# Kernel tuning notes

Measured on AMD Instinct MI355X. Metric: run time of the kernel, lower is better.

Reference implementation:

```python
import jax, jax.numpy as jnp
import numpy as np

D_MODEL, D_STATE, BATCH, SEQ = 512, 32, 8, 4096

def _hippo(n):
    i = np.arange(n)[:, None].astype(np.float64)
    j = np.arange(n)[None, :].astype(np.float64)
    P = np.where(i > j, np.sqrt(2 * i + 1) * np.sqrt(2 * j + 1), 0.0)
    P = P + np.diag(np.arange(1, n + 1).astype(np.float64))
    return (-P).astype(np.float32)

def setup_inputs() -> dict:
    key = jax.random.key(0)
    k0, k1, k2, k3 = jax.random.split(key, 4)
    x = jax.random.normal(k0, (BATCH, SEQ, D_MODEL), dtype=jnp.float32)
    A = jnp.asarray(_hippo(D_STATE))
    B = jax.random.normal(k1, (D_STATE, D_MODEL), dtype=jnp.float32) / np.float32(np.sqrt(D_MODEL))
    C = jax.random.normal(k2, (D_MODEL, D_STATE), dtype=jnp.float32) / np.float32(np.sqrt(D_STATE))
    D = jnp.ones((D_MODEL,), dtype=jnp.float32)
    log_dt = jnp.zeros((D_MODEL,), dtype=jnp.float32)
    W_out = jax.random.normal(k3, (D_MODEL, D_MODEL), dtype=jnp.float32) / np.float32(np.sqrt(D_MODEL))
    b_out = jnp.zeros((D_MODEL,), dtype=jnp.float32)
    return {"x": x, "A": A, "B": B, "C": C, "D": D, "log_dt": log_dt, "W_out": W_out, "b_out": b_out}

def reference(x, A, B, C, D, log_dt, W_out, b_out):
    # x: (b, s, d). S4 layer with bilinear discretization and tanh recurrence.
    n = A.shape[0]
    dt = jnp.mean(jnp.clip(jnp.exp(log_dt), 1e-4, 1.0))  # scalar dt.mean()
    I = jnp.eye(n, dtype=x.dtype)
    inv_term = jnp.linalg.inv(I - 0.5 * dt * A)
    A_bar = (I + 0.5 * dt * A) @ inv_term          # (n, n)
    B_bar = dt * (inv_term @ B)                    # (n, d)
    # Precompute input projection for all timesteps (vectorized):
    uB = jnp.einsum('bsd,nd->bsn', x, B_bar)       # (b, s, n)
    s0 = jnp.zeros((x.shape[0], n), dtype=x.dtype)
    def step(state, ub_t):
        state = jnp.tanh(state @ A_bar.T + ub_t)   # (b, n)
        return state, state
    final_state, states = jax.lax.scan(step, s0, jnp.swapaxes(uB, 0, 1))
    states = jnp.swapaxes(states, 0, 1)            # (b, s, n)
    y = jnp.einsum('bsn,dn->bsd', states, C) + x * D
    y = y @ W_out.T + b_out                        # output_proj (dropout = eval identity)
    return y, final_state
```

## Files before the change

### kernel.cpp

```cpp
#include <hip/hip_runtime.h>
#include <hip/hip_bf16.h>

#define D_MODEL 512
#define D_STATE 32
#define BATCH 8
#define SEQ 4096
#define MROWS (BATCH * SEQ)

typedef __bf16 bf16;
typedef __bf16 bf16x4 __attribute__((ext_vector_type(4)));
typedef __bf16 bf16x8 __attribute__((ext_vector_type(8)));
typedef float f32x4 __attribute__((ext_vector_type(4)));

#define CHUNK 16
#define BURN 80
#define NCHUNK (SEQ / CHUNK)

__device__ __forceinline__ bf16x8 cvt8(const f32x4 a, const f32x4 b) {
  bf16x8 h;
  h[0] = (bf16)a[0]; h[1] = (bf16)a[1]; h[2] = (bf16)a[2]; h[3] = (bf16)a[3];
  h[4] = (bf16)b[0]; h[5] = (bf16)b[1]; h[6] = (bf16)b[2]; h[7] = (bf16)b[3];
  return h;
}

__global__ __launch_bounds__(256) void k_pre(
    const float* __restrict__ A, const float* __restrict__ C, const float* __restrict__ Dv,
    const float* __restrict__ log_dt, const float* __restrict__ W,
    float* __restrict__ A_bar, float* __restrict__ XTs,
    bf16* __restrict__ CW, bf16* __restrict__ WD) {
  __shared__ float Xs[32][32];
  const int bid = blockIdx.x, t = threadIdx.x;
  float* Xf = &Xs[0][0];

  if (bid == 0) {
    {
      float v0 = __expf(log_dt[t]);
      float v1 = __expf(log_dt[t + 256]);
      v0 = fminf(fmaxf(v0, 1e-4f), 1.0f);
      v1 = fminf(fmaxf(v1, 1e-4f), 1.0f);
      Xf[t] = v0 + v1;
    }
    __syncthreads();
    for (int s2 = 128; s2 > 0; s2 >>= 1) {
      if (t < s2) Xf[t] += Xf[t + s2];
      __syncthreads();
    }
    const float dtv = Xf[0] * (1.0f / 512.0f);
    __syncthreads();
    {
      const int i0 = 4 * t;
      const f32x4 av = *(const f32x4*)(A + i0);
      f32x4 mv;
#pragma unroll
      for (int q = 0; q < 4; q++) {
        const int r = (i0 + q) >> 5, c = (i0 + q) & 31;
        mv[q] = (r == c ? 1.0f : 0.0f) - 0.5f * dtv * av[q];
      }
      *(f32x4*)(Xf + i0) = mv;
    }
    __syncthreads();
    if (t < 32) {
      const int j = t;
      float xcol[32];
#pragma unroll
      for (int i = 0; i < 32; i++) {
        float s0 = 0.f, s1 = 0.f, s2 = 0.f, s3 = 0.f;
#pragma unroll
        for (int k = 0; k < 32; k += 4) {
          if (k < i)     s0 -= Xf[i * 32 + k]     * xcol[k];
          if (k + 1 < i) s1 -= Xf[i * 32 + k + 1] * xcol[k + 1];
          if (k + 2 < i) s2 -= Xf[i * 32 + k + 2] * xcol[k + 2];
          if (k + 3 < i) s3 -= Xf[i * 32 + k + 3] * xcol[k + 3];
        }
        const float num = (i == j ? 1.0f : 0.0f) + ((s0 + s1) + (s2 + s3));
        xcol[i] = (i >= j) ? num / Xf[i * 32 + i] : 0.0f;
      }
#pragma unroll
      for (int i = 0; i < 32; i++) Xs[i][j] = xcol[i];
    }
    __syncthreads();
    {
      const int i0 = 4 * t;
      const int r = t >> 3;
      f32x4 ov;
#pragma unroll
      for (int q = 0; q < 4; q++) {
        const int c = (i0 + q) & 31;
        float s = 0.f;
#pragma unroll
        for (int k = 0; k < 32; k++) {
          const float p2 = (r == k ? 1.0f : 0.0f) + 0.5f * dtv * A[r * 32 + k];
          s = fmaf(p2, Xf[k * 32 + c], s);
        }
        ov[q] = s;
      }
      *(f32x4*)(A_bar + i0) = ov;
    }
#pragma unroll
    for (int i = 0; i < 4; i++) {
      const int idx = t + i * 256;
      const int k = idx >> 5, n = idx & 31;
      XTs[idx] = dtv * Xf[n * 32 + k];
    }
  } else if (bid <= 16) {
    const int w = t >> 6, lane = t & 63;
    const int l15 = lane & 15, kg = lane >> 4;
    const int m = w & 1, nf = w >> 1;
    const int eb = (bid - 1) * 32;
    const float* wp = W + (long)(eb + m * 16 + l15) * D_MODEL + kg * 8;
    const int ncol = nf * 16 + l15;
    f32x4 acc = (f32x4)(0.0f);
#pragma unroll 1
    for (int kt = 0; kt < 16; kt++) {
      const f32x4 w0 = *(const f32x4*)(wp + kt * 32);
      const f32x4 w1 = *(const f32x4*)(wp + kt * 32 + 4);
      const bf16x8 af = cvt8(w0, w1);
      bf16x8 bf;
#pragma unroll
      for (int j = 0; j < 8; j++)
        bf[j] = (bf16)C[(kt * 32 + kg * 8 + j) * D_STATE + ncol];
      acc = __builtin_amdgcn_mfma_f32_16x16x32_bf16(af, bf, acc, 0, 0, 0);
    }
#pragma unroll
    for (int jj = 0; jj < 4; jj++)
      CW[(eb + m * 16 + kg * 4 + jj) * D_STATE + ncol] = (bf16)acc[jj];
  } else {
#pragma unroll
    for (int jj = 0; jj < 16; jj++) {
      const int i = (bid - 17) * 16384 + jj * 1024 + t * 4;
      const f32x4 wv = *(const f32x4*)(W + i);
      const f32x4 dv = *(const f32x4*)(Dv + (i & 511));
      bf16x4 h;
#pragma unroll
      for (int q = 0; q < 4; q++) h[q] = (bf16)(wv[q] * dv[q]);
      *(bf16x4*)(WD + i) = h;
    }
  }
}

__device__ __forceinline__ void stage_x(const float* __restrict__ x, long rowbase,
                                        int kt, void* lds, int t) {
#pragma unroll
  for (int j = 0; j < 2; j++) {
    const int boff = j * 4096 + t * 16;
    const int r = boff >> 7;
    const int s = (boff >> 4) & 7;
    const int cb = (s ^ (r & 7)) << 4;
    const char* src = (const char*)(x + (rowbase + r) * D_MODEL) + kt * 128 + cb;
    const int udst = j * 4096 + ((t >> 6) << 10);
    __builtin_amdgcn_global_load_lds(
        (const __attribute__((address_space(1))) void*)src,
        (__attribute__((address_space(3))) void*)((char*)lds + udst), 16, 0, 0);
  }
}

__global__ __launch_bounds__(256, 2) void k_uB(
    const float* __restrict__ x, const float* __restrict__ B,
    const float* __restrict__ XTs,
    float* __restrict__ uB, bf16* __restrict__ xb) {
  __shared__ float xs[2][64 * 32];
  __shared__ float sXT[1024];
  __shared__ float srw[64 * 33];
  const int t = threadIdx.x, w = t >> 6, lane = t & 63;
  const int l15 = lane & 15, kg = lane >> 4;
  const long rowbase = (long)blockIdx.x * 64;

#pragma unroll
  for (int i = 0; i < 4; i++) sXT[t + i * 256] = XTs[t + i * 256];

  const int arow = w * 16 + l15;
  bf16* xo = xb + (rowbase + arow) * D_MODEL + kg * 8;
  const float* bp0 = B + l15 * D_MODEL + kg * 8;
  const float* bp1 = B + (16 + l15) * D_MODEL + kg * 8;
  const int ps0 = (((kg * 2) ^ (arow & 7)) << 2);
  const int ps1 = (((kg * 2 + 1) ^ (arow & 7)) << 2);
  const float* xsrow0 = &xs[0][arow * 32];
  const float* xsrow1 = &xs[1][arow * 32];

  f32x4 acc0 = (f32x4)(0.0f), acc1 = (f32x4)(0.0f);
  f32x4 cb0, cb1, cb2, cb3, nb0, nb1, nb2, nb3;

  stage_x(x, rowbase, 0, &xs[0][0], t);
  cb0 = *(const f32x4*)(bp0); cb1 = *(const f32x4*)(bp0 + 4);
  cb2 = *(const f32x4*)(bp1); cb3 = *(const f32x4*)(bp1 + 4);

#pragma unroll 1
  for (int kt = 0; kt < 16; kt++) {
    __syncthreads();
    if (kt < 15) {
      stage_x(x, rowbase, kt + 1, &xs[(kt + 1) & 1][0], t);
      const int o = (kt + 1) * 32;
      nb0 = *(const f32x4*)(bp0 + o); nb1 = *(const f32x4*)(bp0 + o + 4);
      nb2 = *(const f32x4*)(bp1 + o); nb3 = *(const f32x4*)(bp1 + o + 4);
    }
    const float* xr = (kt & 1) ? xsrow1 : xsrow0;
    const f32x4 a0 = *(const f32x4*)(xr + ps0);
    const f32x4 a1 = *(const f32x4*)(xr + ps1);
    const bf16x8 af = cvt8(a0, a1);
    *(bf16x8*)(xo + kt * 32) = af;
    const bf16x8 bh0 = cvt8(cb0, cb1);
    const bf16x8 bh1 = cvt8(cb2, cb3);
    bf16x8 bl0, bl1;
#pragma unroll
    for (int q = 0; q < 4; q++) {
      bl0[q]     = (bf16)(cb0[q] - (float)bh0[q]);
      bl0[q + 4] = (bf16)(cb1[q] - (float)bh0[q + 4]);
      bl1[q]     = (bf16)(cb2[q] - (float)bh1[q]);
      bl1[q + 4] = (bf16)(cb3[q] - (float)bh1[q + 4]);
    }
    acc0 = __builtin_amdgcn_mfma_f32_16x16x32_bf16(af, bh0, acc0, 0, 0, 0);
    acc0 = __builtin_amdgcn_mfma_f32_16x16x32_bf16(af, bl0, acc0, 0, 0, 0);
    acc1 = __builtin_amdgcn_mfma_f32_16x16x32_bf16(af, bh1, acc1, 0, 0, 0);
    acc1 = __builtin_amdgcn_mfma_f32_16x16x32_bf16(af, bl1, acc1, 0, 0, 0);
    cb0 = nb0; cb1 = nb1; cb2 = nb2; cb3 = nb3;
  }
#pragma unroll
  for (int jj = 0; jj < 4; jj++) {
    srw[(w * 16 + kg * 4 + jj) * 33 + l15]      = acc0[jj];
    srw[(w * 16 + kg * 4 + jj) * 33 + 16 + l15] = acc1[jj];
  }
  __syncthreads();
  {
    const int r = t & 63, ng = t >> 6;
    f32x4 u0 = (f32x4)(0.0f), u1 = (f32x4)(0.0f);
#pragma unroll
    for (int k = 0; k < 32; k++) {
      const float sv = srw[r * 33 + k];
      const f32x4 x0 = *(const f32x4*)&sXT[k * 32 + ng * 4];
      const f32x4 x1 = *(const f32x4*)&sXT[k * 32 + ng * 4 + 16];
#pragma unroll
      for (int q = 0; q < 4; q++) {
        u0[q] = fmaf(sv, x0[q], u0[q]);
        u1[q] = fmaf(sv, x1[q], u1[q]);
      }
    }
    float* up = uB + (rowbase + r) * D_STATE;
    *(f32x4*)(up + ng * 4) = u0;
    *(f32x4*)(up + ng * 4 + 16) = u1;
  }
}

__global__ void k_scan(const float* __restrict__ uB, const float* __restrict__ A_bar,
                       bf16* __restrict__ Sb, float* __restrict__ fs) {
  __shared__ float sbuf[256];
  const int t = threadIdx.x;
  const int g = t >> 5, n = t & 31;
  const int chain = blockIdx.x * 8 + g;
  const int b = chain >> 8;
  const int ch = chain & 255;
  const int cs = ch * CHUNK;
  const int t0 = cs - BURN;
  const int ce = cs + CHUNK;

  float a[32];
#pragma unroll
  for (int k = 0; k < 32; k += 4) {
    const f32x4 v = *(const f32x4*)(A_bar + n * 32 + k);
    a[k] = v[0]; a[k + 1] = v[1]; a[k + 2] = v[2]; a[k + 3] = v[3];
  }
#pragma unroll
  for (int k = 0; k < 32; k++) asm volatile("" : "+v"(a[k]));

  const float* ub = uB + (long)b * SEQ * D_STATE + n;
  bf16* sp = Sb + ((long)b * SEQ + cs) * D_STATE + n;
  float* myslot = &sbuf[g * 32];

  float s = 0.f;
  float ubuf[8], unext[8];
#pragma unroll
  for (int i = 0; i < 8; i++) {
    const int tt = t0 + i;
    ubuf[i] = (tt >= 0) ? ub[(long)tt * D_STATE] : 0.f;
  }
  for (int tg = t0; tg < ce; tg += 8) {
    const int tn = tg + 8;
#pragma unroll
    for (int i = 0; i < 8; i++) {
      const int tt = tn + i;
      unext[i] = (tt >= 0 && tt < ce) ? ub[(long)tt * D_STATE] : 0.f;
    }
#pragma unroll
    for (int i = 0; i < 8; i++) {
      const int tt = tg + i;
      myslot[n] = s;
      const f32x4 s0 = *(const f32x4*)(myslot + 0);
      const f32x4 s1 = *(const f32x4*)(myslot + 4);
      const f32x4 s2 = *(const f32x4*)(myslot + 8);
      const f32x4 s3 = *(const f32x4*)(myslot + 12);
      const f32x4 s4 = *(const f32x4*)(myslot + 16);
      const f32x4 s5 = *(const f32x4*)(myslot + 20);
      const f32x4 s6 = *(const f32x4*)(myslot + 24);
      const f32x4 s7 = *(const f32x4*)(myslot + 28);
      float acc0 = ubuf[i], acc1 = 0.f, acc2 = 0.f, acc3 = 0.f;
#pragma unroll
      for (int q = 0; q < 4; q++) {
        acc0 = fmaf(a[0 + q],  s0[q], acc0);
        acc1 = fmaf(a[4 + q],  s1[q], acc1);
        acc2 = fmaf(a[8 + q],  s2[q], acc2);
        acc3 = fmaf(a[12 + q], s3[q], acc3);
        acc0 = fmaf(a[16 + q], s4[q], acc0);
        acc1 = fmaf(a[20 + q], s5[q], acc1);
        acc2 = fmaf(a[24 + q], s6[q], acc2);
        acc3 = fmaf(a[28 + q], s7[q], acc3);
      }
      const float z = (acc0 + acc1) + (acc2 + acc3);
      const float e = __expf(2.f * z);
      const float r = __builtin_amdgcn_rcpf(e + 1.f);
      s = fmaf(-2.f, r, 1.f);
      if (tt >= cs) sp[(long)(tt - cs) * D_STATE] = (bf16)s;
    }
#pragma unroll
    for (int i = 0; i < 8; i++) ubuf[i] = unext[i];
  }
  if (ch == NCHUNK - 1) fs[b * D_STATE + n] = s;
}

__device__ __forceinline__ void stage_tile(const void* gbase, long row0, long rowStrideB,
                                           int kByte, void* lds, int w, int lane) {
#pragma unroll
  for (int j = 0; j < 2; j++) {
    const int base_off = (w << 11) + (j << 10);
    const int boff = base_off + (lane << 4);
    const int r = boff >> 6;
    const int s = (boff >> 4) & 3;
    const int cb = ((s ^ (r & 3)) << 4);
    const char* src = (const char*)gbase + (row0 + r) * rowStrideB + kByte + cb;
    __builtin_amdgcn_global_load_lds(
        (const __attribute__((address_space(1))) void*)src,
        (__attribute__((address_space(3))) void*)((char*)lds + base_off), 16, 0, 0);
  }
}

__global__ __launch_bounds__(256) void k_out(const bf16* __restrict__ xb,
                                             const bf16* __restrict__ WD,
                                             const bf16* __restrict__ Sb,
                                             const bf16* __restrict__ CW,
                                             const float* __restrict__ bias,
                                             float* __restrict__ out) {
  __shared__ bf16 As[2][128 * 32];
  __shared__ bf16 Bs[2][128 * 32];
  const int tid = threadIdx.x;
  const int w = tid >> 6, lane = tid & 63;
  const int swz = (blockIdx.x & 7) * 128 + (blockIdx.x >> 3);
  const int bm = swz >> 2, bn = swz & 3;
  const long rowbase = (long)bm * 128;
  const long colbase = (long)bn * 128;
  const int wr = w >> 1, wc = w & 1;
  const int l15 = lane & 15, kg = lane >> 4;
  const int kgs = kg ^ (l15 & 3);

  f32x4 acc[4][4];
#pragma unroll
  for (int m = 0; m < 4; m++)
#pragma unroll
    for (int n = 0; n < 4; n++) acc[m][n] = (f32x4)(0.0f);

  const int aoff = (wr * 64 + l15) * 32 + kgs * 8;
  const int boff = (wc * 64 + l15) * 32 + kgs * 8;

  auto STAGE = [&](int ti, int b) {
    if (ti < 16) {
      stage_tile(xb, rowbase, 1024, ti * 64, &As[b][0], w, lane);
      stage_tile(WD, colbase, 1024, ti * 64, &Bs[b][0], w, lane);
    } else {
      stage_tile(Sb, rowbase, 64, 0, &As[b][0], w, lane);
      stage_tile(CW, colbase, 64, 0, &Bs[b][0], w, lane);
    }
  };

  STAGE(0, 0);
  __syncthreads();
#pragma unroll 1
  for (int kt = 0; kt < 17; kt++) {
    const int cur = kt & 1;
    if (kt < 16) STAGE(kt + 1, cur ^ 1);
    bf16x8 af[4], bfr[4];
#pragma unroll
    for (int m = 0; m < 4; m++) af[m] = *(const bf16x8*)&As[cur][aoff + m * 16 * 32];
#pragma unroll
    for (int n = 0; n < 4; n++) bfr[n] = *(const bf16x8*)&Bs[cur][boff + n * 16 * 32];
#pragma unroll
    for (int m = 0; m < 4; m++)
#pragma unroll
      for (int n = 0; n < 4; n++)
        acc[m][n] = __builtin_amdgcn_mfma_f32_16x16x32_bf16(af[m], bfr[n], acc[m][n], 0, 0, 0);
    __syncthreads();
  }
#pragma unroll
  for (int n = 0; n < 4; n++) {
    const int e = (int)colbase + wc * 64 + n * 16 + l15;
    const float bv = bias[e];
#pragma unroll
    for (int m = 0; m < 4; m++) {
      const long r0 = rowbase + wr * 64 + m * 16 + kg * 4;
      const f32x4 v = acc[m][n];
#pragma unroll
      for (int jj = 0; jj < 4; jj++) out[(r0 + jj) * (long)D_MODEL + e] = v[jj] + bv;
    }
  }
}

extern "C" void kernel_launch(void* const* d_in, const int* in_sizes, int n_in,
                              void* d_out, int out_size, void* d_ws, size_t ws_size,
                              hipStream_t stream) {
  const float* x      = (const float*)d_in[0];
  const float* A      = (const float*)d_in[1];
  const float* B      = (const float*)d_in[2];
  const float* C      = (const float*)d_in[3];
  const float* Dv     = (const float*)d_in[4];
  const float* log_dt = (const float*)d_in[5];
  const float* W      = (const float*)d_in[6];
  const float* b_out  = (const float*)d_in[7];
  float* out = (float*)d_out;
  float* fs  = out + (long)MROWS * D_MODEL;

  char* ws = (char*)d_ws;
  float* A_bar = (float*)(ws + 0);
  float* XTs   = (float*)(ws + (4L << 10));
  bf16*  CW    = (bf16*)(ws + (68L << 10));
  bf16*  WD    = (bf16*)(ws + (100L << 10));
  bf16*  Sb    = (bf16*)(ws + (612L << 10));
  float* uB    = (float*)(ws + (2660L << 10));
  bf16*  xb    = (bf16*)(ws + (6756L << 10));

  k_pre<<<dim3(33), dim3(256), 0, stream>>>(A, C, Dv, log_dt, W, A_bar, XTs, CW, WD);
  k_uB<<<dim3(MROWS / 64), dim3(256), 0, stream>>>(x, B, XTs, uB, xb);
  k_scan<<<dim3(256), dim3(256), 0, stream>>>(uB, A_bar, Sb, fs);
  k_out<<<dim3((MROWS / 128) * (D_MODEL / 128)), dim3(256), 0, stream>>>(xb, WD, Sb, CW, b_out, out);
}
```

Baseline: 91.22 us.

## Use fp16 dot2 in scan, widen output GEMM tile, raise uB occupancy

The scan kernel now keeps A_bar and the shared state in fp16 and uses packed fdot2 instructions, which halves the LDS traffic and the FMA count per recurrence step. The output GEMM tile grows from 128x128 to 128x256 per block to improve operand reuse, at the cost of more accumulator registers and fewer blocks. k_uB launch bounds now request 4 blocks per CU. The fp16 state and A_bar values lower the precision of the tanh recurrence.

```diff
diff --git a/kernel.cpp b/kernel.cpp
--- a/kernel.cpp
+++ b/kernel.cpp
@@ -11,6 +11,9 @@
 typedef __bf16 bf16x4 __attribute__((ext_vector_type(4)));
 typedef __bf16 bf16x8 __attribute__((ext_vector_type(8)));
 typedef float f32x4 __attribute__((ext_vector_type(4)));
+typedef _Float16 half_t;
+typedef _Float16 half2_t __attribute__((ext_vector_type(2)));
+typedef _Float16 half8 __attribute__((ext_vector_type(8)));
 
 #define CHUNK 16
 #define BURN 80
@@ -154,7 +157,7 @@
   }
 }
 
-__global__ __launch_bounds__(256, 2) void k_uB(
+__global__ __launch_bounds__(256, 4) void k_uB(
     const float* __restrict__ x, const float* __restrict__ B,
     const float* __restrict__ XTs,
     float* __restrict__ uB, bf16* __restrict__ xb) {
@@ -242,7 +245,7 @@
 
 __global__ void k_scan(const float* __restrict__ uB, const float* __restrict__ A_bar,
                        bf16* __restrict__ Sb, float* __restrict__ fs) {
-  __shared__ float sbuf[256];
+  __shared__ half_t hs[256];
   const int t = threadIdx.x;
   const int g = t >> 5, n = t & 31;
   const int chain = blockIdx.x * 8 + g;
@@ -252,18 +255,18 @@
   const int t0 = cs - BURN;
   const int ce = cs + CHUNK;
 
-  float a[32];
-#pragma unroll
-  for (int k = 0; k < 32; k += 4) {
-    const f32x4 v = *(const f32x4*)(A_bar + n * 32 + k);
-    a[k] = v[0]; a[k + 1] = v[1]; a[k + 2] = v[2]; a[k + 3] = v[3];
-  }
-#pragma unroll
-  for (int k = 0; k < 32; k++) asm volatile("" : "+v"(a[k]));
+  half2_t ah[16];
+#pragma unroll
+  for (int k = 0; k < 16; k++) {
+    ah[k][0] = (half_t)A_bar[n * 32 + 2 * k];
+    ah[k][1] = (half_t)A_bar[n * 32 + 2 * k + 1];
+  }
+#pragma unroll
+  for (int k = 0; k < 16; k++) asm volatile("" : "+v"(ah[k]));
 
   const float* ub = uB + (long)b * SEQ * D_STATE + n;
   bf16* sp = Sb + ((long)b * SEQ + cs) * D_STATE + n;
-  float* myslot = &sbuf[g * 32];
+  half_t* myslot = &hs[g * 32];
 
   float s = 0.f;
   float ubuf[8], unext[8];
@@ -282,27 +285,32 @@
 #pragma unroll
     for (int i = 0; i < 8; i++) {
       const int tt = tg + i;
-      myslot[n] = s;
-      const f32x4 s0 = *(const f32x4*)(myslot + 0);
-      const f32x4 s1 = *(const f32x4*)(myslot + 4);
-      const f32x4 s2 = *(const f32x4*)(myslot + 8);
-      const f32x4 s3 = *(const f32x4*)(myslot + 12);
-      const f32x4 s4 = *(const f32x4*)(myslot + 16);
-      const f32x4 s5 = *(const f32x4*)(myslot + 20);
-      const f32x4 s6 = *(const f32x4*)(myslot + 24);
-      const f32x4 s7 = *(const f32x4*)(myslot + 28);
+      myslot[n] = (half_t)s;
+      const half8 h0 = *(const half8*)(myslot + 0);
+      const half8 h1 = *(const half8*)(myslot + 8);
+      const half8 h2 = *(const half8*)(myslot + 16);
+      const half8 h3 = *(const half8*)(myslot + 24);
       float acc0 = ubuf[i], acc1 = 0.f, acc2 = 0.f, acc3 = 0.f;
-#pragma unroll
-      for (int q = 0; q < 4; q++) {
-        acc0 = fmaf(a[0 + q],  s0[q], acc0);
-        acc1 = fmaf(a[4 + q],  s1[q], acc1);
-        acc2 = fmaf(a[8 + q],  s2[q], acc2);
-        acc3 = fmaf(a[12 + q], s3[q], acc3);
-        acc0 = fmaf(a[16 + q], s4[q], acc0);
-        acc1 = fmaf(a[20 + q], s5[q], acc1);
-        acc2 = fmaf(a[24 + q], s6[q], acc2);
-        acc3 = fmaf(a[28 + q], s7[q], acc3);
-      }
+#if __has_builtin(__builtin_amdgcn_fdot2)
+#pragma unroll
+      for (int j = 0; j < 4; j++) {
+        acc0 = __builtin_amdgcn_fdot2(ah[j],      ((const half2_t*)&h0)[j], acc0, false);
+        acc1 = __builtin_amdgcn_fdot2(ah[4 + j],  ((const half2_t*)&h1)[j], acc1, false);
+        acc2 = __builtin_amdgcn_fdot2(ah[8 + j],  ((const half2_t*)&h2)[j], acc2, false);
+        acc3 = __builtin_amdgcn_fdot2(ah[12 + j], ((const half2_t*)&h3)[j], acc3, false);
+      }
+#else
+#pragma unroll
+      for (int j = 0; j < 4; j++) {
+#pragma unroll
+        for (int q = 0; q < 2; q++) {
+          acc0 = fmaf((float)ah[j][q],      (float)((const half2_t*)&h0)[j][q], acc0);
+          acc1 = fmaf((float)ah[4 + j][q],  (float)((const half2_t*)&h1)[j][q], acc1);
+          acc2 = fmaf((float)ah[8 + j][q],  (float)((const half2_t*)&h2)[j][q], acc2);
+          acc3 = fmaf((float)ah[12 + j][q], (float)((const half2_t*)&h3)[j][q], acc3);
+        }
+      }
+#endif
       const float z = (acc0 + acc1) + (acc2 + acc3);
       const float e = __expf(2.f * z);
       const float r = __builtin_amdgcn_rcpf(e + 1.f);
@@ -315,8 +323,8 @@
   if (ch == NCHUNK - 1) fs[b * D_STATE + n] = s;
 }
 
-__device__ __forceinline__ void stage_tile(const void* gbase, long row0, long rowStrideB,
-                                           int kByte, void* lds, int w, int lane) {
+__device__ __forceinline__ void stage_tile8(const void* gbase, long row0, long rowStrideB,
+                                            int kByte, void* lds, int w, int lane) {
 #pragma unroll
   for (int j = 0; j < 2; j++) {
     const int base_off = (w << 11) + (j << 10);
@@ -331,6 +339,22 @@
   }
 }
 
+__device__ __forceinline__ void stage_tile16(const void* gbase, long row0, long rowStrideB,
+                                             int kByte, void* lds, int w, int lane) {
+#pragma unroll
+  for (int j = 0; j < 4; j++) {
+    const int base_off = (w << 12) + (j << 10);
+    const int boff = base_off + (lane << 4);
+    const int r = boff >> 6;
+    const int s = (boff >> 4) & 3;
+    const int cb = ((s ^ (r & 3)) << 4);
+    const char* src = (const char*)gbase + (row0 + r) * rowStrideB + kByte + cb;
+    __builtin_amdgcn_global_load_lds(
+        (const __attribute__((address_space(1))) void*)src,
+        (__attribute__((address_space(3))) void*)((char*)lds + base_off), 16, 0, 0);
+  }
+}
+
 __global__ __launch_bounds__(256) void k_out(const bf16* __restrict__ xb,
                                              const bf16* __restrict__ WD,
                                              const bf16* __restrict__ Sb,
@@ -338,33 +362,33 @@
                                              const float* __restrict__ bias,
                                              float* __restrict__ out) {
   __shared__ bf16 As[2][128 * 32];
-  __shared__ bf16 Bs[2][128 * 32];
+  __shared__ bf16 Bs[2][256 * 32];
   const int tid = threadIdx.x;
   const int w = tid >> 6, lane = tid & 63;
-  const int swz = (blockIdx.x & 7) * 128 + (blockIdx.x >> 3);
-  const int bm = swz >> 2, bn = swz & 3;
+  const int swz = (blockIdx.x & 7) * 64 + (blockIdx.x >> 3);
+  const int bm = swz >> 1, bn = swz & 1;
   const long rowbase = (long)bm * 128;
-  const long colbase = (long)bn * 128;
+  const long colbase = (long)bn * 256;
   const int wr = w >> 1, wc = w & 1;
   const int l15 = lane & 15, kg = lane >> 4;
   const int kgs = kg ^ (l15 & 3);
 
-  f32x4 acc[4][4];
+  f32x4 acc[4][8];
 #pragma unroll
   for (int m = 0; m < 4; m++)
 #pragma unroll
-    for (int n = 0; n < 4; n++) acc[m][n] = (f32x4)(0.0f);
+    for (int n = 0; n < 8; n++) acc[m][n] = (f32x4)(0.0f);
 
   const int aoff = (wr * 64 + l15) * 32 + kgs * 8;
-  const int boff = (wc * 64 + l15) * 32 + kgs * 8;
+  const int boff = (wc * 128 + l15) * 32 + kgs * 8;
 
   auto STAGE = [&](int ti, int b) {
     if (ti < 16) {
-      stage_tile(xb, rowbase, 1024, ti * 64, &As[b][0], w, lane);
-      stage_tile(WD, colbase, 1024, ti * 64, &Bs[b][0], w, lane);
+      stage_tile8(xb, rowbase, 1024, ti * 64, &As[b][0], w, lane);
+      stage_tile16(WD, colbase, 1024, ti * 64, &Bs[b][0], w, lane);
     } else {
-      stage_tile(Sb, rowbase, 64, 0, &As[b][0], w, lane);
-      stage_tile(CW, colbase, 64, 0, &Bs[b][0], w, lane);
+      stage_tile8(Sb, rowbase, 64, 0, &As[b][0], w, lane);
+      stage_tile16(CW, colbase, 64, 0, &Bs[b][0], w, lane);
     }
   };
 
@@ -374,21 +398,21 @@
   for (int kt = 0; kt < 17; kt++) {
     const int cur = kt & 1;
     if (kt < 16) STAGE(kt + 1, cur ^ 1);
-    bf16x8 af[4], bfr[4];
+    bf16x8 af[4], bfr[8];
 #pragma unroll
     for (int m = 0; m < 4; m++) af[m] = *(const bf16x8*)&As[cur][aoff + m * 16 * 32];
 #pragma unroll
-    for (int n = 0; n < 4; n++) bfr[n] = *(const bf16x8*)&Bs[cur][boff + n * 16 * 32];
+    for (int n = 0; n < 8; n++) bfr[n] = *(const bf16x8*)&Bs[cur][boff + n * 16 * 32];
 #pragma unroll
     for (int m = 0; m < 4; m++)
 #pragma unroll
-      for (int n = 0; n < 4; n++)
+      for (int n = 0; n < 8; n++)
         acc[m][n] = __builtin_amdgcn_mfma_f32_16x16x32_bf16(af[m], bfr[n], acc[m][n], 0, 0, 0);
     __syncthreads();
   }
 #pragma unroll
-  for (int n = 0; n < 4; n++) {
-    const int e = (int)colbase + wc * 64 + n * 16 + l15;
+  for (int n = 0; n < 8; n++) {
+    const int e = (int)colbase + wc * 128 + n * 16 + l15;
     const float bv = bias[e];
 #pragma unroll
     for (int m = 0; m < 4; m++) {
@@ -426,5 +450,5 @@
   k_pre<<<dim3(33), dim3(256), 0, stream>>>(A, C, Dv, log_dt, W, A_bar, XTs, CW, WD);
   k_uB<<<dim3(MROWS / 64), dim3(256), 0, stream>>>(x, B, XTs, uB, xb);
   k_scan<<<dim3(256), dim3(256), 0, stream>>>(uB, A_bar, Sb, fs);
-  k_out<<<dim3((MROWS / 128) * (D_MODEL / 128)), dim3(256), 0, stream>>>(xb, WD, Sb, CW, b_out, out);
-}
+  k_out<<<dim3((MROWS / 128) * (D_MODEL / 256)), dim3(256), 0, stream>>>(xb, WD, Sb, CW, b_out, out);
+}
```

Result: slower. 101.9 us (+11.7%).
